# Kernel tuning notes

Hardware: AMD Instinct MI355X
Metric: run time of the kernel (lower is better)

## Reference

```python
import jax, jax.numpy as jnp
import numpy as np

B = 1024       # batch of triples
E = 50000      # num_entities
R = 500        # num_relations
D = 512        # dimension
P = 16         # parts
C = 8          # num_cores
ALPHA = 2.0    # -> q = alpha/2 = 1.0
Q = ALPHA / 2.0
DP = D // P    # 32


def setup_inputs() -> dict:
    key = jax.random.key(0)
    ks = jax.random.split(key, 10)
    xav_e = (2.0 / (E + D)) ** 0.5
    xav_r = (2.0 / (R + D)) ** 0.5
    return {
        "heads": jax.random.randint(ks[0], (B,), 0, E),
        "relations": jax.random.randint(ks[1], (B,), 0, R),
        "tails": jax.random.randint(ks[2], (B,), 0, E),
        "entity_w": jax.random.normal(ks[3], (E, D), dtype=jnp.float32) * xav_e,
        "relation_w": jax.random.normal(ks[4], (R, D), dtype=jnp.float32) * xav_r,
        "W_cores": jax.random.uniform(ks[5], (C, P, P, P), dtype=jnp.float32,
                                      minval=-0.01, maxval=0.01),
        "attn_w1": jax.random.normal(ks[6], (2 * D, D), dtype=jnp.float32) * (1.0 / (2 * D)) ** 0.5,
        "attn_b1": jnp.zeros((D,), dtype=jnp.float32),
        "attn_w2": jax.random.normal(ks[7], (D, C), dtype=jnp.float32) * (1.0 / D) ** 0.5,
        "attn_b2": jnp.zeros((C,), dtype=jnp.float32),
    }


def _pq_norm(x):
    # ((|x|^p).sum(2) ** q).sum(1), p=2
    return ((x * x).sum(2) ** Q).sum(1)


def _geometric_consistency(W_cores):
    # center of mass of |W| along each axis, per core; vectorized over cores
    coords = jnp.arange(P, dtype=jnp.float32)
    Wa = jnp.abs(W_cores)                      # [C,P,P,P]
    tot = Wa.sum(axis=(1, 2, 3))               # [C]
    cx = (Wa * coords[None, :, None, None]).sum(axis=(1, 2, 3)) / tot
    cy = (Wa * coords[None, None, :, None]).sum(axis=(1, 2, 3)) / tot
    cz = (Wa * coords[None, None, None, :]).sum(axis=(1, 2, 3)) / tot
    centers = jnp.stack([cx, cy, cz], axis=1)  # [C,3]
    d2 = ((centers[:, None, :] - centers[None, :, :]) ** 2).sum(-1)
    dist = jnp.sqrt(d2)
    masked = dist + jnp.eye(C, dtype=dist.dtype) * 1e6
    min_d = masked.min(axis=1)
    return -jnp.mean(jnp.log(min_d + 1e-6))


def reference(heads, relations, tails, entity_w, relation_w, W_cores,
              attn_w1, attn_b1, attn_w2, attn_b2):
    h = entity_w[heads]          # [B,D]
    r = relation_w[relations]    # [B,D]
    t = entity_w[tails]          # [B,D]

    hr = jnp.concatenate([h, r], axis=1)                       # [B,2D]
    hid = jax.nn.relu(hr @ attn_w1 + attn_b1)                  # [B,D]
    attn = jax.nn.softmax(hid @ attn_w2 + attn_b2, axis=1)     # [B,C]

    h3 = h.reshape(-1, DP, P)
    r3 = r.reshape(-1, DP, P)
    t3 = t.reshape(-1, DP, P)

    h_norm = _pq_norm(h3)
    r_norm = _pq_norm(r3)
    t_norm = _pq_norm(t3)

    # attention-weighted effective core per triple (sum over cores is linear,
    # so folding attn into W before the contraction is exactly the same math)
    Weff = jnp.einsum('bc,cpqs->bpqs', attn, W_cores)          # [B,P,P,P]

    # x1[b,i,s] = sum_{p,q} h[b,i,p] r[b,i,q] W[b,p,q,s]
    x1 = jnp.einsum('bip,biq,bpqs->bis', h3, r3, Weff)
    # x2[b,i,p] = sum_{q,s} r[b,i,q] t[b,i,s] W[b,p,q,s]
    x2 = jnp.einsum('biq,bis,bpqs->bip', r3, t3, Weff)
    # x3[b,i,q] = sum_{p,s} h[b,i,p] t[b,i,s] W[b,p,q,s]
    x3 = jnp.einsum('bip,bis,bpqs->biq', h3, t3, Weff)

    whr_norm = _pq_norm(x1)
    wrt_norm = _pq_norm(x2)
    wth_norm = _pq_norm(x3)

    scores = x1.reshape(-1, D) @ entity_w.T                    # [B,E]

    factor1 = jnp.mean(h_norm) + jnp.mean(r_norm) + jnp.mean(t_norm)
    factor2 = jnp.mean(whr_norm) + jnp.mean(wrt_norm) + jnp.mean(wth_norm)
    factor3 = _geometric_consistency(W_cores)
    return (scores, factor1, factor2, factor3, attn)
```

## Files before the change

kernel.cpp:

```cpp
#include <hip/hip_runtime.h>
#include <cstdint>
#include <cstddef>

#define NB 1024
#define NE 50000
#define NE_PAD 50048
#define DCOL 512
#define ATTN_C 8

static const size_t SCORES_OFF = (size_t)NB * NE;
static const size_t F1_OFF = SCORES_OFF + 0;
static const size_t F2_OFF = SCORES_OFF + 1;
static const size_t F3_OFF = SCORES_OFF + 2;
static const size_t ATTN_OFF = SCORES_OFF + 3;

typedef float f32x4 __attribute__((ext_vector_type(4)));
typedef short s16x8 __attribute__((ext_vector_type(8)));

__device__ __forceinline__ unsigned short f2bf(float f) {
  union { float f; uint32_t u; } x; x.f = f;
  uint32_t u = x.u;
  uint32_t r = (u + 0x7fffu + ((u >> 16) & 1u)) >> 16;
  return (unsigned short)r;
}

__device__ __forceinline__ void gload16(const void* g, void* l) {
  __builtin_amdgcn_global_load_lds(
      (const __attribute__((address_space(1))) uint32_t*)g,
      (__attribute__((address_space(3))) uint32_t*)l, 16, 0, 0);
}

template <int N>
__device__ __forceinline__ void waitcnt_vm() {
  static_assert(N == 0 || N == 4 || N == 8, "literal dispatch");
  if constexpr (N == 0) asm volatile("s_waitcnt vmcnt(0)" ::: "memory");
  else if constexpr (N == 4) asm volatile("s_waitcnt vmcnt(4)" ::: "memory");
  else if constexpr (N == 8) asm volatile("s_waitcnt vmcnt(8)" ::: "memory");
}

__global__ __launch_bounds__(256)
void prep(const int* __restrict__ heads, const int* __restrict__ rels,
          const int* __restrict__ tails, const float* __restrict__ ew,
          const float* __restrict__ rw, const float* __restrict__ w1,
          unsigned short* __restrict__ hrb, unsigned short* __restrict__ w1t,
          unsigned short* __restrict__ ewb, float* __restrict__ n1) {
  int tid = threadIdx.x;
  if (blockIdx.x < NB) {
    int b = blockIdx.x;
    const float* h = ew + (size_t)heads[b] * DCOL;
    const float* r = rw + (size_t)rels[b] * DCOL;
    const float* t = ew + (size_t)tails[b] * DCOL;
    float acc = 0.f;
    #pragma unroll
    for (int it = 0; it < 2; ++it) {
      int d = it * 256 + tid;
      float hv = h[d], rv = r[d], tv = t[d];
      hrb[(size_t)b * 1024 + d] = f2bf(hv);
      hrb[(size_t)b * 1024 + DCOL + d] = f2bf(rv);
      acc += hv * hv + rv * rv + tv * tv;
    }
    __shared__ float red[256];
    red[tid] = acc; __syncthreads();
    for (int s = 128; s > 0; s >>= 1) {
      if (tid < s) red[tid] += red[tid + s];
      __syncthreads();
    }
    if (tid == 0) n1[b] = red[0];
  } else if (blockIdx.x < NB + 512) {
    int tb = blockIdx.x - NB;
    int nb = (tb & 15) * 32, kb = (tb >> 4) * 32;
    __shared__ float tile[32][33];
    int tx = tid & 31, ty = tid >> 5;
    #pragma unroll
    for (int rr = 0; rr < 32; rr += 8)
      tile[ty + rr][tx] = w1[(size_t)(kb + ty + rr) * 512 + nb + tx];
    __syncthreads();
    #pragma unroll
    for (int rr = 0; rr < 32; rr += 8)
      w1t[(size_t)(nb + ty + rr) * 1024 + kb + tx] = f2bf(tile[tx][ty + rr]);
  } else {
    const int n4valid = NE * DCOL / 4;
    const int n4tot = NE_PAD * DCOL / 4;
    int i = (blockIdx.x - NB - 512) * 256 + tid;
    const int stride = 2048 * 256;
    for (; i < n4tot; i += stride) {
      float x = 0.f, y = 0.f, z = 0.f, w = 0.f;
      if (i < n4valid) {
        float4 v = ((const float4*)ew)[i];
        x = v.x; y = v.y; z = v.z; w = v.w;
      }
      union { unsigned short u[4]; uint2 v2; } o;
      o.u[0] = f2bf(x); o.u[1] = f2bf(y); o.u[2] = f2bf(z); o.u[3] = f2bf(w);
      ((uint2*)ewb)[i] = o.v2;
    }
  }
}

template <int EPI, int FR, int SWZ, int MT>
__global__ __launch_bounds__(256, 2)
void gemm_nt(const unsigned short* __restrict__ A,
             const unsigned short* __restrict__ B,
             float* __restrict__ C, const float* __restrict__ bias,
             int K, int Nc, int NT) {
  constexpr int BM = FR * 32;
  constexpr int TILE = BM * 128;
  __shared__ __align__(16) uint8_t smem[4 * TILE];
  const int tid = threadIdx.x;
  const int lane = tid & 63;
  const int wv = tid >> 6;
  const int wm = wv >> 1, wn = wv & 1;

  int m_t, n_t;
  if (SWZ) {
    int xcd = blockIdx.x & 7;
    int l = blockIdx.x >> 3;
    int w = xcd * ((MT * NT) >> 3) + l;
    n_t = w / MT; m_t = w % MT;
  } else {
    m_t = blockIdx.x % MT; n_t = blockIdx.x / MT;
  }
  const int m0 = m_t * BM;
  const int n0 = n_t * BM;
  const int rbytes = K * 2;

  f32x4 acc[FR][FR];
  #pragma unroll
  for (int i = 0; i < FR; ++i)
    #pragma unroll
    for (int j = 0; j < FR; ++j) acc[i][j] = (f32x4){0.f, 0.f, 0.f, 0.f};

  const int srow = lane >> 3;
  const int scol = lane & 7;
  const int nkt = K >> 6;

  auto stage = [&](int kt, int buf) {
    #pragma unroll
    for (int j = 0; j < FR; ++j) {
      const int chunk = wv * FR + j;
      const int r = chunk * 8 + srow;
      const int c = scol ^ (r & 7);
      gload16((const uint8_t*)A + (size_t)(m0 + r) * rbytes + kt * 128 + c * 16,
              &smem[buf * 2 * TILE + chunk * 1024]);
      gload16((const uint8_t*)B + (size_t)(n0 + r) * rbytes + kt * 128 + c * 16,
              &smem[buf * 2 * TILE + TILE + chunk * 1024]);
    }
  };
  auto compute = [&](int buf) {
    const uint8_t* sa = &smem[buf * 2 * TILE];
    const uint8_t* sb = sa + TILE;
    #pragma unroll
    for (int kk = 0; kk < 2; ++kk) {
      s16x8 af[FR], bfv[FR];
      #pragma unroll
      for (int f = 0; f < FR; ++f) {
        const int ra = wm * 16 * FR + f * 16 + (lane & 15);
        const int ca = (kk * 4 + (lane >> 4)) ^ (ra & 7);
        af[f] = *(const s16x8*)&sa[ra * 128 + ca * 16];
        const int rb = wn * 16 * FR + f * 16 + (lane & 15);
        const int cb = (kk * 4 + (lane >> 4)) ^ (rb & 7);
        bfv[f] = *(const s16x8*)&sb[rb * 128 + cb * 16];
      }
      #pragma unroll
      for (int fm = 0; fm < FR; ++fm)
        #pragma unroll
        for (int fn = 0; fn < FR; ++fn)
          acc[fm][fn] = __builtin_amdgcn_mfma_f32_16x16x32_bf16(
              af[fm], bfv[fn], acc[fm][fn], 0, 0, 0);
    }
  };

  stage(0, 0);
  stage(1, 1);
  for (int kt = 0; kt < nkt - 1; ++kt) {
    const int cur = kt & 1;
    waitcnt_vm<2 * FR>();
    __builtin_amdgcn_sched_barrier(0);
    __builtin_amdgcn_s_barrier();
    __builtin_amdgcn_sched_barrier(0);
    compute(cur);
    __builtin_amdgcn_sched_barrier(0);
    __builtin_amdgcn_s_barrier();
    __builtin_amdgcn_sched_barrier(0);
    if (kt + 2 < nkt) stage(kt + 2, cur);
  }
  waitcnt_vm<0>();
  __builtin_amdgcn_sched_barrier(0);
  __builtin_amdgcn_s_barrier();
  __builtin_amdgcn_sched_barrier(0);
  compute((nkt - 1) & 1);

  const int rl = lane >> 4, cl = lane & 15;
  #pragma unroll
  for (int fm = 0; fm < FR; ++fm)
    #pragma unroll
    for (int fn = 0; fn < FR; ++fn)
      #pragma unroll
      for (int j = 0; j < 4; ++j) {
        int gm = m0 + wm * 16 * FR + fm * 16 + rl * 4 + j;
        int gn = n0 + wn * 16 * FR + fn * 16 + cl;
        if (gn < Nc) {
          float v = acc[fm][fn][j];
          if (EPI) v = fmaxf(v + bias[gn], 0.f);
          C[(size_t)gm * Nc + gn] = v;
        }
      }
}

__global__ __launch_bounds__(256, 2)
void triple_core(const int* __restrict__ heads, const int* __restrict__ rels,
                 const int* __restrict__ tails, const float* __restrict__ ew,
                 const float* __restrict__ rw, const float* __restrict__ wc,
                 const float* __restrict__ hid, const float* __restrict__ w2,
                 const float* __restrict__ b2, float* __restrict__ attn_out,
                 unsigned short* __restrict__ x1b, float* __restrict__ n2) {
  __shared__ float hs[512], rs[512], ts[512];
  __shared__ __align__(16) float W123[4096][4];
  __shared__ float att[8];
  __shared__ float wred[4][8];
  __shared__ float red[256];
  int b = blockIdx.x, tid = threadIdx.x;
  int lane = tid & 63, wid = tid >> 6;
  const float* hp_ = ew + (size_t)heads[b] * DCOL;
  const float* rp_ = rw + (size_t)rels[b] * DCOL;
  const float* tp_ = ew + (size_t)tails[b] * DCOL;
  float la[8] = {0, 0, 0, 0, 0, 0, 0, 0};
  #pragma unroll
  for (int it = 0; it < 2; ++it) {
    int d = it * 256 + tid;
    hs[d] = hp_[d]; rs[d] = rp_[d]; ts[d] = tp_[d];
    float hv = hid[(size_t)b * DCOL + d];
    #pragma unroll
    for (int c = 0; c < 8; ++c) la[c] = fmaf(hv, w2[d * 8 + c], la[c]);
  }
  #pragma unroll
  for (int off = 32; off > 0; off >>= 1)
    #pragma unroll
    for (int c = 0; c < 8; ++c) la[c] += __shfl_down(la[c], off);
  if (lane == 0)
    #pragma unroll
    for (int c = 0; c < 8; ++c) wred[wid][c] = la[c];
  __syncthreads();
  if (tid == 0) {
    float lg[8];
    #pragma unroll
    for (int c = 0; c < 8; ++c)
      lg[c] = wred[0][c] + wred[1][c] + wred[2][c] + wred[3][c] + b2[c];
    float mx = lg[0];
    #pragma unroll
    for (int c = 1; c < 8; ++c) mx = fmaxf(mx, lg[c]);
    float e[8], s = 0.f;
    #pragma unroll
    for (int c = 0; c < 8; ++c) { e[c] = expf(lg[c] - mx); s += e[c]; }
    #pragma unroll
    for (int c = 0; c < 8; ++c) {
      float a = e[c] / s;
      att[c] = a;
      attn_out[(size_t)b * 8 + c] = a;
    }
  }
  __syncthreads();
  #pragma unroll
  for (int it = 0; it < 16; ++it) {
    int idx = it * 256 + tid;
    float w = 0.f;
    #pragma unroll
    for (int c = 0; c < 8; ++c) w = fmaf(att[c], wc[c * 4096 + idx], w);
    int s = idx & 15, q = (idx >> 4) & 15, p = idx >> 8;
    W123[idx][0] = w;
    W123[(q * 16 + s) * 16 + p][1] = w;
    W123[(p * 16 + s) * 16 + q][2] = w;
  }
  __syncthreads();

  const int so = tid & 15;
  const int i0 = tid >> 4, i1 = i0 + 16;
  float h0[16], r0[16], t0[16], h1[16], r1[16], t1[16];
  #pragma unroll
  for (int k = 0; k < 16; ++k) {
    h0[k] = hs[i0 * 16 + k]; r0[k] = rs[i0 * 16 + k]; t0[k] = ts[i0 * 16 + k];
    h1[k] = hs[i1 * 16 + k]; r1[k] = rs[i1 * 16 + k]; t1[k] = ts[i1 * 16 + k];
  }
  float a10 = 0.f, a20 = 0.f, a30 = 0.f, a11 = 0.f, a21 = 0.f, a31 = 0.f;
  const float4* wp = (const float4*)&W123[so][0];
  #pragma unroll
  for (int u = 0; u < 16; ++u) {
    #pragma unroll
    for (int v = 0; v < 16; ++v) {
      float4 w = wp[u * 256 + v * 16];
      a10 = fmaf(h0[u] * r0[v], w.x, a10);
      a20 = fmaf(r0[u] * t0[v], w.y, a20);
      a30 = fmaf(h0[u] * t0[v], w.z, a30);
      a11 = fmaf(h1[u] * r1[v], w.x, a11);
      a21 = fmaf(r1[u] * t1[v], w.y, a21);
      a31 = fmaf(h1[u] * t1[v], w.z, a31);
    }
  }
  x1b[(size_t)b * 512 + i0 * 16 + so] = f2bf(a10);
  x1b[(size_t)b * 512 + i1 * 16 + so] = f2bf(a11);
  red[tid] = a10 * a10 + a20 * a20 + a30 * a30
           + a11 * a11 + a21 * a21 + a31 * a31;
  __syncthreads();
  for (int s = 128; s > 0; s >>= 1) {
    if (tid < s) red[tid] += red[tid + s];
    __syncthreads();
  }
  if (tid == 0) n2[b] = red[0];
}

__global__ __launch_bounds__(256)
void finalize(const float* __restrict__ n1, const float* __restrict__ n2,
              const float* __restrict__ wc, float* __restrict__ out) {
  int tid = threadIdx.x;
  __shared__ float red[256];
  float a = 0.f;
  for (int i = tid; i < NB; i += 256) a += n1[i];
  red[tid] = a; __syncthreads();
  for (int s = 128; s > 0; s >>= 1) { if (tid < s) red[tid] += red[tid + s]; __syncthreads(); }
  if (tid == 0) out[F1_OFF] = red[0] / (float)NB;
  __syncthreads();
  a = 0.f;
  for (int i = tid; i < NB; i += 256) a += n2[i];
  red[tid] = a; __syncthreads();
  for (int s = 128; s > 0; s >>= 1) { if (tid < s) red[tid] += red[tid + s]; __syncthreads(); }
  if (tid == 0) out[F2_OFF] = red[0] / (float)NB;
  __syncthreads();

  int c = tid >> 5, l = tid & 31;
  float tot = 0.f, cx = 0.f, cy = 0.f, cz = 0.f;
  for (int e = l; e < 4096; e += 32) {
    float w = fabsf(wc[c * 4096 + e]);
    int z = e & 15, y = (e >> 4) & 15, x = e >> 8;
    tot += w; cx += w * x; cy += w * y; cz += w * z;
  }
  #pragma unroll
  for (int off = 16; off > 0; off >>= 1) {
    tot += __shfl_down(tot, off);
    cx += __shfl_down(cx, off);
    cy += __shfl_down(cy, off);
    cz += __shfl_down(cz, off);
  }
  __shared__ float cent[8][3];
  if (l == 0) { cent[c][0] = cx / tot; cent[c][1] = cy / tot; cent[c][2] = cz / tot; }
  __syncthreads();
  if (tid == 0) {
    float f3 = 0.f;
    for (int i = 0; i < 8; ++i) {
      float mn = 1e30f;
      for (int j = 0; j < 8; ++j) {
        if (j == i) continue;
        float dx = cent[i][0] - cent[j][0];
        float dy = cent[i][1] - cent[j][1];
        float dz = cent[i][2] - cent[j][2];
        float d = sqrtf(dx * dx + dy * dy + dz * dz);
        mn = fminf(mn, d);
      }
      f3 += logf(mn + 1e-6f);
    }
    out[F3_OFF] = -f3 / 8.f;
  }
}

extern "C" void kernel_launch(void* const* d_in, const int* in_sizes, int n_in,
                              void* d_out, int out_size, void* d_ws, size_t ws_size,
                              hipStream_t stream) {
  const int* heads = (const int*)d_in[0];
  const int* rels = (const int*)d_in[1];
  const int* tails = (const int*)d_in[2];
  const float* ew = (const float*)d_in[3];
  const float* rw = (const float*)d_in[4];
  const float* wc = (const float*)d_in[5];
  const float* w1 = (const float*)d_in[6];
  const float* b1 = (const float*)d_in[7];
  const float* w2 = (const float*)d_in[8];
  const float* b2 = (const float*)d_in[9];
  float* out = (float*)d_out;

  uint8_t* ws = (uint8_t*)d_ws;
  const size_t EWB_SZ = (size_t)NE_PAD * DCOL * 2;
  unsigned short* ewb = (unsigned short*)ws;
  unsigned short* hrb = (unsigned short*)(ws + EWB_SZ);
  unsigned short* w1t = (unsigned short*)(ws + EWB_SZ + 2097152);
  float* hid = (float*)(ws + EWB_SZ + 2097152 + 1048576);
  unsigned short* x1b = (unsigned short*)(ws + EWB_SZ + 2097152 + 1048576 + 2097152);
  float* n1 = (float*)(ws + EWB_SZ + 2097152 + 1048576 + 2097152 + 1048576);
  float* n2 = n1 + NB;

  prep<<<NB + 512 + 2048, 256, 0, stream>>>(heads, rels, tails, ew, rw, w1,
                                            hrb, w1t, ewb, n1);
  gemm_nt<1, 2, 0, 16><<<128, 256, 0, stream>>>(
      hrb, w1t, hid, b1, 1024, 512, 8);
  triple_core<<<NB, 256, 0, stream>>>(heads, rels, tails, ew, rw, wc,
                                      hid, w2, b2, out + ATTN_OFF, x1b, n2);
  gemm_nt<0, 4, 1, 8><<<3128, 256, 0, stream>>>(
      x1b, ewb, out, nullptr, 512, NE, 391);
  finalize<<<1, 256, 0, stream>>>(n1, n2, wc, out);
}
```

Measured before the change: 212.3 us.

## Fuse entity-table bf16 conversion into scores GEMM B-tile loading

After: 243.5 us. +14.7%, slower.

```diff
diff --git a/kernel.cpp b/kernel.cpp
--- a/kernel.cpp
+++ b/kernel.cpp
@@ -4,7 +4,6 @@
 
 #define NB 1024
 #define NE 50000
-#define NE_PAD 50048
 #define DCOL 512
 #define ATTN_C 8
 
@@ -32,10 +31,11 @@
 
 template <int N>
 __device__ __forceinline__ void waitcnt_vm() {
-  static_assert(N == 0 || N == 4 || N == 8, "literal dispatch");
+  static_assert(N == 0 || N == 4 || N == 8 || N == 12, "literal dispatch");
   if constexpr (N == 0) asm volatile("s_waitcnt vmcnt(0)" ::: "memory");
   else if constexpr (N == 4) asm volatile("s_waitcnt vmcnt(4)" ::: "memory");
   else if constexpr (N == 8) asm volatile("s_waitcnt vmcnt(8)" ::: "memory");
+  else if constexpr (N == 12) asm volatile("s_waitcnt vmcnt(12)" ::: "memory");
 }
 
 __global__ __launch_bounds__(256)
@@ -43,7 +43,7 @@
           const int* __restrict__ tails, const float* __restrict__ ew,
           const float* __restrict__ rw, const float* __restrict__ w1,
           unsigned short* __restrict__ hrb, unsigned short* __restrict__ w1t,
-          unsigned short* __restrict__ ewb, float* __restrict__ n1) {
+          float* __restrict__ n1) {
   int tid = threadIdx.x;
   if (blockIdx.x < NB) {
     int b = blockIdx.x;
@@ -66,7 +66,7 @@
       __syncthreads();
     }
     if (tid == 0) n1[b] = red[0];
-  } else if (blockIdx.x < NB + 512) {
+  } else {
     int tb = blockIdx.x - NB;
     int nb = (tb & 15) * 32, kb = (tb >> 4) * 32;
     __shared__ float tile[32][33];
@@ -78,32 +78,21 @@
     #pragma unroll
     for (int rr = 0; rr < 32; rr += 8)
       w1t[(size_t)(nb + ty + rr) * 1024 + kb + tx] = f2bf(tile[tx][ty + rr]);
-  } else {
-    const int n4valid = NE * DCOL / 4;
-    const int n4tot = NE_PAD * DCOL / 4;
-    int i = (blockIdx.x - NB - 512) * 256 + tid;
-    const int stride = 2048 * 256;
-    for (; i < n4tot; i += stride) {
-      float x = 0.f, y = 0.f, z = 0.f, w = 0.f;
-      if (i < n4valid) {
-        float4 v = ((const float4*)ew)[i];
-        x = v.x; y = v.y; z = v.z; w = v.w;
-      }
-      union { unsigned short u[4]; uint2 v2; } o;
-      o.u[0] = f2bf(x); o.u[1] = f2bf(y); o.u[2] = f2bf(z); o.u[3] = f2bf(w);
-      ((uint2*)ewb)[i] = o.v2;
-    }
-  }
-}
-
-template <int EPI, int FR, int SWZ, int MT>
+  }
+}
+
+template <int EPI, int FR, int SWZ, int MT, int KTOT, int BF32>
 __global__ __launch_bounds__(256, 2)
 void gemm_nt(const unsigned short* __restrict__ A,
-             const unsigned short* __restrict__ B,
+             const unsigned short* __restrict__ Bb,
+             const float* __restrict__ Bf,
              float* __restrict__ C, const float* __restrict__ bias,
-             int K, int Nc, int NT) {
+             int Nc, int NrowsB, int NT) {
   constexpr int BM = FR * 32;
   constexpr int TILE = BM * 128;
+  constexpr int NKT = KTOT / 64;
+  constexpr int SOPS = BF32 ? 3 * FR : 2 * FR;
+  static_assert(NKT % 2 == 0, "unroll-by-2 assumes even K-tile count");
   __shared__ __align__(16) uint8_t smem[4 * TILE];
   const int tid = threadIdx.x;
   const int lane = tid & 63;
@@ -121,7 +110,7 @@
   }
   const int m0 = m_t * BM;
   const int n0 = n_t * BM;
-  const int rbytes = K * 2;
+  constexpr int RBY = KTOT * 2;
 
   f32x4 acc[FR][FR];
   #pragma unroll
@@ -131,18 +120,48 @@
 
   const int srow = lane >> 3;
   const int scol = lane & 7;
-  const int nkt = K >> 6;
-
-  auto stage = [&](int kt, int buf) {
+
+  auto stageA = [&](int kt, int buf) {
     #pragma unroll
     for (int j = 0; j < FR; ++j) {
       const int chunk = wv * FR + j;
       const int r = chunk * 8 + srow;
       const int c = scol ^ (r & 7);
-      gload16((const uint8_t*)A + (size_t)(m0 + r) * rbytes + kt * 128 + c * 16,
+      gload16((const uint8_t*)A + (size_t)(m0 + r) * RBY + kt * 128 + c * 16,
               &smem[buf * 2 * TILE + chunk * 1024]);
-      gload16((const uint8_t*)B + (size_t)(n0 + r) * rbytes + kt * 128 + c * 16,
+    }
+  };
+  auto stageBb = [&](int kt, int buf) {
+    #pragma unroll
+    for (int j = 0; j < FR; ++j) {
+      const int chunk = wv * FR + j;
+      const int r = chunk * 8 + srow;
+      const int c = scol ^ (r & 7);
+      gload16((const uint8_t*)Bb + (size_t)(n0 + r) * RBY + kt * 128 + c * 16,
               &smem[buf * 2 * TILE + TILE + chunk * 1024]);
+    }
+  };
+  auto loadB32 = [&](int kt, float4 (&q0)[FR], float4 (&q1)[FR]) {
+    #pragma unroll
+    for (int j = 0; j < FR; ++j) {
+      const int r = (wv * FR + j) * 8 + srow;
+      int rn = n0 + r; rn = rn < NrowsB ? rn : NrowsB - 1;
+      const int c = scol ^ (r & 7);
+      const float* src = Bf + (size_t)rn * KTOT + kt * 64 + c * 8;
+      q0[j] = *(const float4*)src;
+      q1[j] = *(const float4*)(src + 4);
+    }
+  };
+  auto writeB = [&](int buf, float4 (&q0)[FR], float4 (&q1)[FR]) {
+    #pragma unroll
+    for (int j = 0; j < FR; ++j) {
+      const int chunk = wv * FR + j;
+      s16x8 o;
+      o[0] = (short)f2bf(q0[j].x); o[1] = (short)f2bf(q0[j].y);
+      o[2] = (short)f2bf(q0[j].z); o[3] = (short)f2bf(q0[j].w);
+      o[4] = (short)f2bf(q1[j].x); o[5] = (short)f2bf(q1[j].y);
+      o[6] = (short)f2bf(q1[j].z); o[7] = (short)f2bf(q1[j].w);
+      *(s16x8*)&smem[buf * 2 * TILE + TILE + chunk * 1024 + srow * 128 + scol * 16] = o;
     }
   };
   auto compute = [&](int buf) {
@@ -169,25 +188,65 @@
     }
   };
 
-  stage(0, 0);
-  stage(1, 1);
-  for (int kt = 0; kt < nkt - 1; ++kt) {
-    const int cur = kt & 1;
-    waitcnt_vm<2 * FR>();
-    __builtin_amdgcn_sched_barrier(0);
-    __builtin_amdgcn_s_barrier();
-    __builtin_amdgcn_sched_barrier(0);
-    compute(cur);
-    __builtin_amdgcn_sched_barrier(0);
-    __builtin_amdgcn_s_barrier();
-    __builtin_amdgcn_sched_barrier(0);
-    if (kt + 2 < nkt) stage(kt + 2, cur);
-  }
-  waitcnt_vm<0>();
+  float4 pA0[FR], pA1[FR], pB0[FR], pB1[FR];
+
+  stageA(0, 0);
+  if constexpr (BF32) loadB32(0, pA0, pA1); else stageBb(0, 0);
+  stageA(1, 1);
+  if constexpr (BF32) loadB32(1, pB0, pB1); else stageBb(1, 1);
   __builtin_amdgcn_sched_barrier(0);
+  waitcnt_vm<SOPS>();
+  __builtin_amdgcn_sched_barrier(0);
+  if constexpr (BF32) {
+    writeB(0, pA0, pA1);
+    asm volatile("s_waitcnt lgkmcnt(0)" ::: "memory");
+    __builtin_amdgcn_sched_barrier(0);
+  }
   __builtin_amdgcn_s_barrier();
   __builtin_amdgcn_sched_barrier(0);
-  compute((nkt - 1) & 1);
+
+  #pragma unroll
+  for (int k2 = 0; k2 < NKT; k2 += 2) {
+    compute(0);
+    __builtin_amdgcn_sched_barrier(0);
+    __builtin_amdgcn_s_barrier();
+    __builtin_amdgcn_sched_barrier(0);
+    if (k2 + 2 < NKT) {
+      stageA(k2 + 2, 0);
+      if constexpr (BF32) loadB32(k2 + 2, pA0, pA1); else stageBb(k2 + 2, 0);
+    }
+    __builtin_amdgcn_sched_barrier(0);
+    if (k2 + 2 < NKT) waitcnt_vm<SOPS>(); else waitcnt_vm<0>();
+    __builtin_amdgcn_sched_barrier(0);
+    if constexpr (BF32) {
+      writeB(1, pB0, pB1);
+      asm volatile("s_waitcnt lgkmcnt(0)" ::: "memory");
+      __builtin_amdgcn_sched_barrier(0);
+    }
+    __builtin_amdgcn_s_barrier();
+    __builtin_amdgcn_sched_barrier(0);
+
+    compute(1);
+    __builtin_amdgcn_sched_barrier(0);
+    __builtin_amdgcn_s_barrier();
+    __builtin_amdgcn_sched_barrier(0);
+    if (k2 + 3 < NKT) {
+      stageA(k2 + 3, 1);
+      if constexpr (BF32) loadB32(k2 + 3, pB0, pB1); else stageBb(k2 + 3, 1);
+    }
+    __builtin_amdgcn_sched_barrier(0);
+    if (k2 + 3 < NKT) waitcnt_vm<SOPS>(); else waitcnt_vm<0>();
+    __builtin_amdgcn_sched_barrier(0);
+    if constexpr (BF32) {
+      if (k2 + 2 < NKT) {
+        writeB(0, pA0, pA1);
+        asm volatile("s_waitcnt lgkmcnt(0)" ::: "memory");
+        __builtin_amdgcn_sched_barrier(0);
+      }
+    }
+    __builtin_amdgcn_s_barrier();
+    __builtin_amdgcn_sched_barrier(0);
+  }
 
   const int rl = lane >> 4, cl = lane & 15;
   #pragma unroll
@@ -376,22 +435,20 @@
   float* out = (float*)d_out;
 
   uint8_t* ws = (uint8_t*)d_ws;
-  const size_t EWB_SZ = (size_t)NE_PAD * DCOL * 2;
-  unsigned short* ewb = (unsigned short*)ws;
-  unsigned short* hrb = (unsigned short*)(ws + EWB_SZ);
-  unsigned short* w1t = (unsigned short*)(ws + EWB_SZ + 2097152);
-  float* hid = (float*)(ws + EWB_SZ + 2097152 + 1048576);
-  unsigned short* x1b = (unsigned short*)(ws + EWB_SZ + 2097152 + 1048576 + 2097152);
-  float* n1 = (float*)(ws + EWB_SZ + 2097152 + 1048576 + 2097152 + 1048576);
+  unsigned short* hrb = (unsigned short*)ws;
+  unsigned short* w1t = (unsigned short*)(ws + 2097152);
+  float* hid = (float*)(ws + 2097152 + 1048576);
+  unsigned short* x1b = (unsigned short*)(ws + 2097152 + 1048576 + 2097152);
+  float* n1 = (float*)(ws + 2097152 + 1048576 + 2097152 + 1048576);
   float* n2 = n1 + NB;
 
-  prep<<<NB + 512 + 2048, 256, 0, stream>>>(heads, rels, tails, ew, rw, w1,
-                                            hrb, w1t, ewb, n1);
-  gemm_nt<1, 2, 0, 16><<<128, 256, 0, stream>>>(
-      hrb, w1t, hid, b1, 1024, 512, 8);
+  prep<<<NB + 512, 256, 0, stream>>>(heads, rels, tails, ew, rw, w1,
+                                     hrb, w1t, n1);
+  gemm_nt<1, 2, 0, 16, 1024, 0><<<128, 256, 0, stream>>>(
+      hrb, w1t, nullptr, hid, b1, 512, 512, 8);
   triple_core<<<NB, 256, 0, stream>>>(heads, rels, tails, ew, rw, wc,
                                       hid, w2, b2, out + ATTN_OFF, x1b, n2);
-  gemm_nt<0, 4, 1, 8><<<3128, 256, 0, stream>>>(
-      x1b, ewb, out, nullptr, 512, NE, 391);
+  gemm_nt<0, 4, 1, 8, 512, 1><<<3128, 256, 0, stream>>>(
+      x1b, nullptr, ew, out, nullptr, NE, NE, 391);
   finalize<<<1, 256, 0, stream>>>(n1, n2, wc, out);
 }
```

## Make score GEMM persistent with cross-tile prefetch of next tile's K slices

Applied to the files above, without the earlier changes.

Measured after the change: 217.8 us. 1.03x slower.

```diff
diff --git a/kernel.cpp b/kernel.cpp
--- a/kernel.cpp
+++ b/kernel.cpp
@@ -96,32 +96,28 @@
   }
 }
 
-template <int EPI, int FR, int SWZ, int MT>
+template <int EPI, int FR, int MT, int KTOT>
 __global__ __launch_bounds__(256, 2)
 void gemm_nt(const unsigned short* __restrict__ A,
              const unsigned short* __restrict__ B,
              float* __restrict__ C, const float* __restrict__ bias,
-             int K, int Nc, int NT) {
+             int Nc, int total_tiles, int nblocks) {
   constexpr int BM = FR * 32;
   constexpr int TILE = BM * 128;
+  constexpr int NKT = KTOT / 64;
+  constexpr int SOPS = 2 * FR;
   __shared__ __align__(16) uint8_t smem[4 * TILE];
   const int tid = threadIdx.x;
   const int lane = tid & 63;
   const int wv = tid >> 6;
   const int wm = wv >> 1, wn = wv & 1;
-
-  int m_t, n_t;
-  if (SWZ) {
-    int xcd = blockIdx.x & 7;
-    int l = blockIdx.x >> 3;
-    int w = xcd * ((MT * NT) >> 3) + l;
-    n_t = w / MT; m_t = w % MT;
-  } else {
-    m_t = blockIdx.x % MT; n_t = blockIdx.x / MT;
-  }
-  const int m0 = m_t * BM;
-  const int n0 = n_t * BM;
-  const int rbytes = K * 2;
+  constexpr int RBY = KTOT * 2;
+
+  const int per_xcd = total_tiles >> 3;
+  const int xcd = blockIdx.x & 7;
+  const int lstride = nblocks >> 3;
+  int l = blockIdx.x >> 3;
+  if (l >= per_xcd) return;
 
   f32x4 acc[FR][FR];
   #pragma unroll
@@ -131,17 +127,16 @@
 
   const int srow = lane >> 3;
   const int scol = lane & 7;
-  const int nkt = K >> 6;
-
-  auto stage = [&](int kt, int buf) {
+
+  auto stage = [&](int kt, int buf, int m0, int n0) {
     #pragma unroll
     for (int j = 0; j < FR; ++j) {
       const int chunk = wv * FR + j;
       const int r = chunk * 8 + srow;
       const int c = scol ^ (r & 7);
-      gload16((const uint8_t*)A + (size_t)(m0 + r) * rbytes + kt * 128 + c * 16,
+      gload16((const uint8_t*)A + (size_t)(m0 + r) * RBY + kt * 128 + c * 16,
               &smem[buf * 2 * TILE + chunk * 1024]);
-      gload16((const uint8_t*)B + (size_t)(n0 + r) * rbytes + kt * 128 + c * 16,
+      gload16((const uint8_t*)B + (size_t)(n0 + r) * RBY + kt * 128 + c * 16,
               &smem[buf * 2 * TILE + TILE + chunk * 1024]);
     }
   };
@@ -169,41 +164,54 @@
     }
   };
 
-  stage(0, 0);
-  stage(1, 1);
-  for (int kt = 0; kt < nkt - 1; ++kt) {
-    const int cur = kt & 1;
-    waitcnt_vm<2 * FR>();
-    __builtin_amdgcn_sched_barrier(0);
-    __builtin_amdgcn_s_barrier();
-    __builtin_amdgcn_sched_barrier(0);
-    compute(cur);
-    __builtin_amdgcn_sched_barrier(0);
-    __builtin_amdgcn_s_barrier();
-    __builtin_amdgcn_sched_barrier(0);
-    if (kt + 2 < nkt) stage(kt + 2, cur);
-  }
-  waitcnt_vm<0>();
-  __builtin_amdgcn_sched_barrier(0);
-  __builtin_amdgcn_s_barrier();
-  __builtin_amdgcn_sched_barrier(0);
-  compute((nkt - 1) & 1);
+  int w = xcd * per_xcd + l;
+  int m0 = (w % MT) * BM, n0 = (w / MT) * BM;
+  stage(0, 0, m0, n0);
+  stage(1, 1, m0, n0);
 
   const int rl = lane >> 4, cl = lane & 15;
-  #pragma unroll
-  for (int fm = 0; fm < FR; ++fm)
-    #pragma unroll
-    for (int fn = 0; fn < FR; ++fn)
+  while (true) {
+    const int ln = l + lstride;
+    const bool lastt = ln >= per_xcd;
+    int m0n = m0, n0n = n0;
+    if (!lastt) {
+      int wn2 = xcd * per_xcd + ln;
+      m0n = (wn2 % MT) * BM; n0n = (wn2 / MT) * BM;
+    }
+    #pragma unroll
+    for (int k = 0; k < NKT; ++k) {
+      const int c = k & 1;
+      if (lastt && k == NKT - 1) waitcnt_vm<0>();
+      else waitcnt_vm<SOPS>();
+      __builtin_amdgcn_sched_barrier(0);
+      __builtin_amdgcn_s_barrier();
+      __builtin_amdgcn_sched_barrier(0);
+      compute(c);
+      __builtin_amdgcn_sched_barrier(0);
+      __builtin_amdgcn_s_barrier();
+      __builtin_amdgcn_sched_barrier(0);
+      if (k + 2 < NKT) stage(k + 2, c, m0, n0);
+      else if (!lastt) stage(k + 2 - NKT, c, m0n, n0n);
+      __builtin_amdgcn_sched_barrier(0);
+    }
+    #pragma unroll
+    for (int fm = 0; fm < FR; ++fm)
       #pragma unroll
-      for (int j = 0; j < 4; ++j) {
-        int gm = m0 + wm * 16 * FR + fm * 16 + rl * 4 + j;
-        int gn = n0 + wn * 16 * FR + fn * 16 + cl;
-        if (gn < Nc) {
-          float v = acc[fm][fn][j];
-          if (EPI) v = fmaxf(v + bias[gn], 0.f);
-          C[(size_t)gm * Nc + gn] = v;
+      for (int fn = 0; fn < FR; ++fn)
+        #pragma unroll
+        for (int j = 0; j < 4; ++j) {
+          int gm = m0 + wm * 16 * FR + fm * 16 + rl * 4 + j;
+          int gn = n0 + wn * 16 * FR + fn * 16 + cl;
+          if (gn < Nc) {
+            float v = acc[fm][fn][j];
+            if (EPI) v = fmaxf(v + bias[gn], 0.f);
+            C[(size_t)gm * Nc + gn] = v;
+          }
+          acc[fm][fn][j] = 0.f;
         }
-      }
+    if (lastt) break;
+    l = ln; m0 = m0n; n0 = n0n;
+  }
 }
 
 __global__ __launch_bounds__(256, 2)
@@ -387,11 +395,11 @@
 
   prep<<<NB + 512 + 2048, 256, 0, stream>>>(heads, rels, tails, ew, rw, w1,
                                             hrb, w1t, ewb, n1);
-  gemm_nt<1, 2, 0, 16><<<128, 256, 0, stream>>>(
-      hrb, w1t, hid, b1, 1024, 512, 8);
+  gemm_nt<1, 2, 16, 1024><<<128, 256, 0, stream>>>(
+      hrb, w1t, hid, b1, 512, 128, 128);
   triple_core<<<NB, 256, 0, stream>>>(heads, rels, tails, ew, rw, wc,
                                       hid, w2, b2, out + ATTN_OFF, x1b, n2);
-  gemm_nt<0, 4, 1, 8><<<3128, 256, 0, stream>>>(
-      x1b, ewb, out, nullptr, 512, NE, 391);
+  gemm_nt<0, 4, 8, 512><<<512, 256, 0, stream>>>(
+      x1b, ewb, out, nullptr, NE, 3128, 512);
   finalize<<<1, 256, 0, stream>>>(n1, n2, wc, out);
 }
```
